# Optimization experiments

Hardware: AMD Instinct MI355X
Metric: run time of the kernel (lower is better)

## Reference

```python
import jax, jax.numpy as jnp
import numpy as np

IN_FEATURES = 2048
OUT_FEATURES = 2048
BLOCK_SIZE = 16
F_BLOCKS = (OUT_FEATURES + BLOCK_SIZE - 1) // BLOCK_SIZE  # 128
G_BLOCKS = (IN_FEATURES + BLOCK_SIZE - 1) // BLOCK_SIZE   # 128
BATCH = 4096


def setup_inputs() -> dict:
    key = jax.random.key(0)
    k1, k2, k3 = jax.random.split(key, 3)
    x = jax.random.normal(k1, (BATCH, IN_FEATURES), dtype=jnp.float32)
    # Xavier-uniform-ish scale for index vectors viewed as (f*g, block_size)
    limit = np.sqrt(6.0 / (F_BLOCKS * G_BLOCKS + BLOCK_SIZE)).astype(np.float32)
    index_vectors = jax.random.uniform(
        k2, (F_BLOCKS, G_BLOCKS, BLOCK_SIZE), dtype=jnp.float32,
        minval=-limit, maxval=limit)
    b = jax.random.normal(k3, (OUT_FEATURES,), dtype=jnp.float32) * 0.02
    return {"x": x, "index_vectors": index_vectors, "b": b}


def reference(x, index_vectors, b):
    batch = x.shape[0]
    padded_in = G_BLOCKS * BLOCK_SIZE
    padded_out = F_BLOCKS * BLOCK_SIZE
    if x.shape[1] < padded_in:
        x = jnp.pad(x, ((0, 0), (0, padded_in - x.shape[1])))
    x_blocks = x.reshape(batch, G_BLOCKS, BLOCK_SIZE)            # (B, g, b)
    # Batched FFT over all blocks at once (replaces the f*g python loop)
    fft_p = jnp.fft.fft(index_vectors, axis=-1)                  # (f, g, b) complex
    fft_x = jnp.fft.fft(x_blocks, axis=-1)                       # (B, g, b) complex
    # sum_j IFFT(P_ij * X_j) == IFFT(sum_j P_ij * X_j) by linearity of IFFT
    out_fft = jnp.einsum('fgb,Bgb->Bfb', fft_p, fft_x)           # (B, f, b) complex
    out_blocks = jnp.fft.ifft(out_fft, axis=-1).real             # (B, f, b)
    out = out_blocks.reshape(batch, padded_out)
    if padded_out > OUT_FEATURES:
        out = out[:, :OUT_FEATURES]
    return out + b
```

## Files before the change

kernel.cpp:

```cpp
#include <hip/hip_runtime.h>
#include <hip/hip_bf16.h>


#define M_DIM 4096
#define N_DIM 2048
#define K_DIM 2048
#define BK 64
#define NT (K_DIM / BK)
#define BUFSZ 49152

typedef __attribute__((ext_vector_type(8))) short bf16x8;
typedef __attribute__((ext_vector_type(4))) float f32x4;

typedef const __attribute__((address_space(1))) void gvoid_t;
typedef __attribute__((address_space(3))) void lvoid_t;

#define FENCE asm volatile("" ::: "memory")
#define BAR()  do { FENCE; __builtin_amdgcn_s_barrier(); FENCE; } while (0)
#define GLD(src, dst) __builtin_amdgcn_global_load_lds((gvoid_t*)(src), (lvoid_t*)(dst), 16, 0, 0)

#define STAGE_A(dst, src) (GLD((src) + 0 * 64 * K_DIM, (dst) + 0),     \
                           GLD((src) + 1 * 64 * K_DIM, (dst) + 8192),  \
                           GLD((src) + 2 * 64 * K_DIM, (dst) + 16384), \
                           GLD((src) + 3 * 64 * K_DIM, (dst) + 24576))
#define STAGE_B(dst, src) (GLD((src) + 0 * 64 * K_DIM, (dst) + 0),     \
                           GLD((src) + 1 * 64 * K_DIM, (dst) + 8192))

__device__ __forceinline__ unsigned int f2bf(float f) {
  unsigned int u = __float_as_uint(f);
  return (u + 0x7fffu + ((u >> 16) & 1u)) >> 16;
}

__global__ __launch_bounds__(256) void prep_kernel(const float* __restrict__ x,
                                                   const float* __restrict__ iv,
                                                   unsigned short* __restrict__ xb,
                                                   unsigned short* __restrict__ W) {
  int b = blockIdx.x;
  if (b < (M_DIM * K_DIM / 8) / 256) {
    int idx = b * 256 + threadIdx.x;
    const float4* x4 = (const float4*)x;
    float4 a = x4[idx * 2 + 0];
    float4 c = x4[idx * 2 + 1];
    uint4 o;
    o.x = f2bf(a.x) | (f2bf(a.y) << 16);
    o.y = f2bf(a.z) | (f2bf(a.w) << 16);
    o.z = f2bf(c.x) | (f2bf(c.y) << 16);
    o.w = f2bf(c.z) | (f2bf(c.w) << 16);
    ((uint4*)xb)[idx] = o;
  } else {
    int idx = (b - (M_DIM * K_DIM / 8) / 256) * 256 + threadIdx.x;
    int o  = idx >> 8;
    int i0 = (idx & 255) * 8;
    int f = o >> 4, t = o & 15;
    int g = i0 >> 4, u0 = i0 & 15;
    const float* row = iv + (f * 128 + g) * 16;
    unsigned int p[4];
#pragma unroll
    for (int j = 0; j < 4; ++j) {
      unsigned int lo = f2bf(row[(t - (u0 + 2 * j + 0)) & 15]);
      unsigned int hi = f2bf(row[(t - (u0 + 2 * j + 1)) & 15]);
      p[j] = lo | (hi << 16);
    }
    ((uint4*)W)[idx] = make_uint4(p[0], p[1], p[2], p[3]);
  }
}

__global__ __launch_bounds__(512, 2) void gemm_bias_kernel(const unsigned short* __restrict__ A,
                                                           const unsigned short* __restrict__ B,
                                                           const float* __restrict__ bias,
                                                           float* __restrict__ C) {
  __shared__ char lds[3 * BUFSZ];

  const int tid = threadIdx.x;
  const int l   = tid & 63;
  const int w   = tid >> 6;
  const int wm  = w >> 1;
  const int wn  = w & 1;

  const int orig = blockIdx.x;
  const int swz  = (orig & 7) * 32 + (orig >> 3);
  const int bm   = swz >> 4;
  const int bn   = swz & 15;

  f32x4 acc[4][4] = {};

  const int srow  = w * 8 + (l >> 3);
  const int sslot = (l & 7) ^ ((l >> 3) & 7);
  const unsigned short* Asrc0 = A + (size_t)(bm * 256 + srow) * K_DIM + sslot * 8;
  const unsigned short* Bsrc0 = B + (size_t)(bn * 128 + srow) * K_DIM + sslot * 8;

  const int fr = l & 15;
  const int rxor = (l & 7) << 4;
  const int aRow0 = (wm * 64 + fr) * 128;
  const int bRow0 = (wn * 64 + fr) * 128;
  const int swzcol0 = (0 * 64 + (l >> 4) * 16) ^ rxor;
  const int swzcol1 = (1 * 64 + (l >> 4) * 16) ^ rxor;

  bf16x8 fa0[4], fb0[4], fa1[4], fb1[4];

#define LDA(SA, SB, BUF, SWZ)                                           \
  do {                                                                  \
    const char* Ab_ = lds + (BUF) * BUFSZ;                              \
    const char* Bb_ = Ab_ + 32768;                                      \
    _Pragma("unroll")                                                   \
    for (int m = 0; m < 4; ++m)                                         \
      SA[m] = *(const bf16x8*)(Ab_ + aRow0 + m * 2048 + (SWZ));         \
    _Pragma("unroll")                                                   \
    for (int n = 0; n < 4; ++n)                                         \
      SB[n] = *(const bf16x8*)(Bb_ + bRow0 + n * 2048 + (SWZ));         \
  } while (0)

#define MM(SA, SB, CNT)                                                 \
  do {                                                                  \
    asm volatile("s_waitcnt lgkmcnt(" #CNT ")" ::: "memory");           \
    __builtin_amdgcn_sched_barrier(0);                                  \
    __builtin_amdgcn_s_setprio(1);                                      \
    _Pragma("unroll")                                                   \
    for (int m = 0; m < 4; ++m)                                         \
      _Pragma("unroll")                                                 \
      for (int n = 0; n < 4; ++n)                                       \
        acc[m][n] = __builtin_amdgcn_mfma_f32_16x16x32_bf16(SA[m], SB[n], acc[m][n], 0, 0, 0); \
    __builtin_amdgcn_s_setprio(0);                                      \
    __builtin_amdgcn_sched_barrier(0);                                  \
  } while (0)

#define TILE_FULL(CUR, NXT, STG, T)                                     \
  do {                                                                  \
    LDA(fa1, fb1, CUR, swzcol1);                                        \
    STAGE_A(lds + (STG) * BUFSZ + w * 1024, Asrc0 + ((T) + 2) * BK);    \
    MM(fa0, fb0, 8);                                                    \
    asm volatile("s_waitcnt vmcnt(4)" ::: "memory");                    \
    BAR();                                                              \
    LDA(fa0, fb0, NXT, swzcol0);                                        \
    STAGE_B(lds + (STG) * BUFSZ + 32768 + w * 1024, Bsrc0 + ((T) + 2) * BK); \
    MM(fa1, fb1, 8);                                                    \
    BAR();                                                              \
  } while (0)

  STAGE_A(lds + 0 * BUFSZ + w * 1024, Asrc0 + 0 * BK);
  STAGE_B(lds + 0 * BUFSZ + 32768 + w * 1024, Bsrc0 + 0 * BK);
  STAGE_A(lds + 1 * BUFSZ + w * 1024, Asrc0 + 1 * BK);
  STAGE_B(lds + 1 * BUFSZ + 32768 + w * 1024, Bsrc0 + 1 * BK);
  asm volatile("s_waitcnt vmcnt(6)" ::: "memory");
  BAR();
  LDA(fa0, fb0, 0, swzcol0);

  for (int t = 0; t < NT - 2; t += 3) {
    TILE_FULL(0, 1, 2, t);
    TILE_FULL(1, 2, 0, t + 1);
    TILE_FULL(2, 0, 1, t + 2);
  }

  LDA(fa1, fb1, 0, swzcol1);
  MM(fa0, fb0, 8);
  asm volatile("s_waitcnt vmcnt(0)" ::: "memory");
  BAR();
  LDA(fa0, fb0, 1, swzcol0);
  MM(fa1, fb1, 8);
  LDA(fa1, fb1, 1, swzcol1);
  MM(fa0, fb0, 8);
  MM(fa1, fb1, 0);

  const int row0 = bm * 256 + wm * 64 + (l >> 4) * 4;
  const int col0 = bn * 128 + wn * 64 + (l & 15);
#pragma unroll
  for (int n = 0; n < 4; ++n) {
    float bv = bias[col0 + n * 16];
#pragma unroll
    for (int m = 0; m < 4; ++m) {
#pragma unroll
      for (int j = 0; j < 4; ++j) {
        C[(size_t)(row0 + m * 16 + j) * N_DIM + (col0 + n * 16)] = acc[m][n][j] + bv;
      }
    }
  }
#undef TILE_FULL
#undef MM
#undef LDA
}

__global__ __launch_bounds__(256) void fallback_kernel(const float* __restrict__ x,
                                                       const float* __restrict__ iv,
                                                       const float* __restrict__ b,
                                                       float* __restrict__ out) {
  int idx = blockIdx.x * 256 + threadIdx.x;
  int Bn = idx >> 11, o = idx & 2047;
  int f = o >> 4, t = o & 15;
  const float* xr = x + (size_t)Bn * 2048;
  float acc = 0.f;
  for (int g = 0; g < 128; ++g) {
    const float* pr = iv + (f * 128 + g) * 16;
    const float* xg = xr + g * 16;
#pragma unroll
    for (int s = 0; s < 16; ++s) acc += pr[s] * xg[(t - s) & 15];
  }
  out[idx] = acc + b[o];
}

extern "C" void kernel_launch(void* const* d_in, const int* in_sizes, int n_in,
                              void* d_out, int out_size, void* d_ws, size_t ws_size,
                              hipStream_t stream) {
  const float* x    = (const float*)d_in[0];
  const float* iv   = (const float*)d_in[1];
  const float* bias = (const float*)d_in[2];
  float* out = (float*)d_out;

  const size_t xb_bytes = (size_t)M_DIM * K_DIM * 2;
  const size_t w_bytes  = (size_t)N_DIM * K_DIM * 2;
  if (ws_size < xb_bytes + w_bytes) {
    fallback_kernel<<<(M_DIM * N_DIM) / 256, 256, 0, stream>>>(x, iv, bias, out);
    return;
  }

  unsigned short* xb = (unsigned short*)d_ws;
  unsigned short* W  = xb + (size_t)M_DIM * K_DIM;

  const int cvt_blocks = (M_DIM * K_DIM / 8) / 256;
  const int bw_blocks  = (N_DIM * K_DIM / 8) / 256;
  prep_kernel<<<cvt_blocks + bw_blocks, 256, 0, stream>>>(x, iv, xb, W);

  gemm_bias_kernel<<<(M_DIM / 256) * (N_DIM / 128), 512, 0, stream>>>(xb, W, bias, out);
}
```

Before: 55.10 us.

## Switch GEMM to 32x32x16 MFMA with intra-block split-K and LDS reduction

Replaces the 16x16x32 MFMA tiling with 32x32x16 bf16 MFMAs. The 8 waves become a 2x2 output grid with two K-groups that each take half of every 64-wide K tile, and the two partial results are reduced through LDS in the epilogue before bias is added. The main loop is restructured so each iteration issues the A and B stages together and waits once per tile, with a single barrier per tile instead of two. The larger MFMA shape is meant to cut LDS fragment traffic per FLOP and instruction issue overhead. In exchange it adds an LDS reduction pass and barrier at the end and raises accumulator register use per wave.

```diff
diff --git a/kernel.cpp b/kernel.cpp
--- a/kernel.cpp
+++ b/kernel.cpp
@@ -11,6 +11,7 @@
 
 typedef __attribute__((ext_vector_type(8))) short bf16x8;
 typedef __attribute__((ext_vector_type(4))) float f32x4;
+typedef __attribute__((ext_vector_type(16))) float f32x16;
 
 typedef const __attribute__((address_space(1))) void gvoid_t;
 typedef __attribute__((address_space(3))) void lvoid_t;
@@ -74,67 +75,70 @@
   const int tid = threadIdx.x;
   const int l   = tid & 63;
   const int w   = tid >> 6;
-  const int wm  = w >> 1;
+  const int wm  = (w >> 1) & 1;
   const int wn  = w & 1;
+  const int kg  = w >> 2;
 
   const int orig = blockIdx.x;
   const int swz  = (orig & 7) * 32 + (orig >> 3);
   const int bm   = swz >> 4;
   const int bn   = swz & 15;
 
-  f32x4 acc[4][4] = {};
+  f32x16 acc[4][2] = {};
 
   const int srow  = w * 8 + (l >> 3);
   const int sslot = (l & 7) ^ ((l >> 3) & 7);
   const unsigned short* Asrc0 = A + (size_t)(bm * 256 + srow) * K_DIM + sslot * 8;
   const unsigned short* Bsrc0 = B + (size_t)(bn * 128 + srow) * K_DIM + sslot * 8;
 
-  const int fr = l & 15;
   const int rxor = (l & 7) << 4;
-  const int aRow0 = (wm * 64 + fr) * 128;
-  const int bRow0 = (wn * 64 + fr) * 128;
-  const int swzcol0 = (0 * 64 + (l >> 4) * 16) ^ rxor;
-  const int swzcol1 = (1 * 64 + (l >> 4) * 16) ^ rxor;
-
-  bf16x8 fa0[4], fb0[4], fa1[4], fb1[4];
-
-#define LDA(SA, SB, BUF, SWZ)                                           \
+  const int aRowB = (wm * 128 + (l & 31)) * 128;
+  const int bRowB = (wn * 64 + (l & 31)) * 128;
+  const int kc0 = (kg * 64 + 0 * 32 + (l >> 5) * 16) ^ rxor;
+  const int kc1 = (kg * 64 + 1 * 32 + (l >> 5) * 16) ^ rxor;
+
+  bf16x8 fa0[4][2], fb0[2][2], fa1[4][2], fb1[2][2];
+
+#define LDFRAGS(FA, FB, BUFC)                                           \
   do {                                                                  \
-    const char* Ab_ = lds + (BUF) * BUFSZ;                              \
+    const char* Ab_ = lds + (BUFC) * BUFSZ;                             \
     const char* Bb_ = Ab_ + 32768;                                      \
     _Pragma("unroll")                                                   \
-    for (int m = 0; m < 4; ++m)                                         \
-      SA[m] = *(const bf16x8*)(Ab_ + aRow0 + m * 2048 + (SWZ));         \
+    for (int mm = 0; mm < 4; ++mm) {                                    \
+      FA[mm][0] = *(const bf16x8*)(Ab_ + aRowB + mm * 4096 + kc0);      \
+      FA[mm][1] = *(const bf16x8*)(Ab_ + aRowB + mm * 4096 + kc1);      \
+    }                                                                   \
     _Pragma("unroll")                                                   \
-    for (int n = 0; n < 4; ++n)                                         \
-      SB[n] = *(const bf16x8*)(Bb_ + bRow0 + n * 2048 + (SWZ));         \
+    for (int nn = 0; nn < 2; ++nn) {                                    \
+      FB[nn][0] = *(const bf16x8*)(Bb_ + bRowB + nn * 4096 + kc0);      \
+      FB[nn][1] = *(const bf16x8*)(Bb_ + bRowB + nn * 4096 + kc1);      \
+    }                                                                   \
   } while (0)
 
-#define MM(SA, SB, CNT)                                                 \
+#define MFMA16(FA, FB, CNT)                                             \
   do {                                                                  \
     asm volatile("s_waitcnt lgkmcnt(" #CNT ")" ::: "memory");           \
     __builtin_amdgcn_sched_barrier(0);                                  \
     __builtin_amdgcn_s_setprio(1);                                      \
     _Pragma("unroll")                                                   \
-    for (int m = 0; m < 4; ++m)                                         \
+    for (int s = 0; s < 2; ++s)                                         \
       _Pragma("unroll")                                                 \
-      for (int n = 0; n < 4; ++n)                                       \
-        acc[m][n] = __builtin_amdgcn_mfma_f32_16x16x32_bf16(SA[m], SB[n], acc[m][n], 0, 0, 0); \
+      for (int mm = 0; mm < 4; ++mm)                                    \
+        _Pragma("unroll")                                               \
+        for (int nn = 0; nn < 2; ++nn)                                  \
+          acc[mm][nn] = __builtin_amdgcn_mfma_f32_32x32x16_bf16(FA[mm][s], FB[nn][s], acc[mm][nn], 0, 0, 0); \
     __builtin_amdgcn_s_setprio(0);                                      \
     __builtin_amdgcn_sched_barrier(0);                                  \
   } while (0)
 
-#define TILE_FULL(CUR, NXT, STG, T)                                     \
+#define BODY(T, BUF2, BUF1, FAc, FBc, FAn, FBn)                         \
   do {                                                                  \
-    LDA(fa1, fb1, CUR, swzcol1);                                        \
-    STAGE_A(lds + (STG) * BUFSZ + w * 1024, Asrc0 + ((T) + 2) * BK);    \
-    MM(fa0, fb0, 8);                                                    \
-    asm volatile("s_waitcnt vmcnt(4)" ::: "memory");                    \
+    STAGE_A(lds + (BUF2) * BUFSZ + w * 1024, Asrc0 + ((T) + 2) * BK);   \
+    STAGE_B(lds + (BUF2) * BUFSZ + 32768 + w * 1024, Bsrc0 + ((T) + 2) * BK); \
+    asm volatile("s_waitcnt vmcnt(6)" ::: "memory");                    \
     BAR();                                                              \
-    LDA(fa0, fb0, NXT, swzcol0);                                        \
-    STAGE_B(lds + (STG) * BUFSZ + 32768 + w * 1024, Bsrc0 + ((T) + 2) * BK); \
-    MM(fa1, fb1, 8);                                                    \
-    BAR();                                                              \
+    LDFRAGS(FAn, FBn, BUF1);                                            \
+    MFMA16(FAc, FBc, 12);                                               \
   } while (0)
 
   STAGE_A(lds + 0 * BUFSZ + w * 1024, Asrc0 + 0 * BK);
@@ -143,40 +147,73 @@
   STAGE_B(lds + 1 * BUFSZ + 32768 + w * 1024, Bsrc0 + 1 * BK);
   asm volatile("s_waitcnt vmcnt(6)" ::: "memory");
   BAR();
-  LDA(fa0, fb0, 0, swzcol0);
-
-  for (int t = 0; t < NT - 2; t += 3) {
-    TILE_FULL(0, 1, 2, t);
-    TILE_FULL(1, 2, 0, t + 1);
-    TILE_FULL(2, 0, 1, t + 2);
-  }
-
-  LDA(fa1, fb1, 0, swzcol1);
-  MM(fa0, fb0, 8);
+  LDFRAGS(fa0, fb0, 0);
+
+  for (int t = 0; t < NT - 2; t += 6) {
+    BODY(t + 0, 2, 1, fa0, fb0, fa1, fb1);
+    BODY(t + 1, 0, 2, fa1, fb1, fa0, fb0);
+    BODY(t + 2, 1, 0, fa0, fb0, fa1, fb1);
+    BODY(t + 3, 2, 1, fa1, fb1, fa0, fb0);
+    BODY(t + 4, 0, 2, fa0, fb0, fa1, fb1);
+    BODY(t + 5, 1, 0, fa1, fb1, fa0, fb0);
+  }
+
   asm volatile("s_waitcnt vmcnt(0)" ::: "memory");
   BAR();
-  LDA(fa0, fb0, 1, swzcol0);
-  MM(fa1, fb1, 8);
-  LDA(fa1, fb1, 1, swzcol1);
-  MM(fa0, fb0, 8);
-  MM(fa1, fb1, 0);
-
-  const int row0 = bm * 256 + wm * 64 + (l >> 4) * 4;
-  const int col0 = bn * 128 + wn * 64 + (l & 15);
-#pragma unroll
-  for (int n = 0; n < 4; ++n) {
-    float bv = bias[col0 + n * 16];
-#pragma unroll
-    for (int m = 0; m < 4; ++m) {
-#pragma unroll
-      for (int j = 0; j < 4; ++j) {
-        C[(size_t)(row0 + m * 16 + j) * N_DIM + (col0 + n * 16)] = acc[m][n][j] + bv;
+  LDFRAGS(fa1, fb1, 1);
+  MFMA16(fa0, fb0, 12);
+  MFMA16(fa1, fb1, 0);
+
+  BAR();
+  {
+    const int p = w & 3;
+    float* rb = (float*)lds + (size_t)p * 2 * 64 * 68;
+    float* mysub  = rb + (kg ? 0 : 1) * 64 * 68;
+    float* othsub = rb + (kg ? 1 : 0) * 64 * 68;
+    const int mmw0 = kg ? 0 : 2;
+    const int mmk0 = kg ? 2 : 0;
+#pragma unroll
+    for (int mi = 0; mi < 2; ++mi)
+#pragma unroll
+      for (int nn = 0; nn < 2; ++nn)
+#pragma unroll
+        for (int q = 0; q < 4; ++q) {
+          const int rloc = mi * 32 + q * 8 + (l >> 5) * 4;
+          const int col  = nn * 32 + (l & 31);
+          f32x4 v;
+          v[0] = acc[mmw0 + mi][nn][q * 4 + 0];
+          v[1] = acc[mmw0 + mi][nn][q * 4 + 1];
+          v[2] = acc[mmw0 + mi][nn][q * 4 + 2];
+          v[3] = acc[mmw0 + mi][nn][q * 4 + 3];
+          *(f32x4*)(mysub + col * 68 + rloc) = v;
+        }
+    asm volatile("s_waitcnt lgkmcnt(0)" ::: "memory");
+    BAR();
+    const int col0 = bn * 128 + wn * 64;
+#pragma unroll
+    for (int nn = 0; nn < 2; ++nn) {
+      const float bv = bias[col0 + nn * 32 + (l & 31)];
+#pragma unroll
+      for (int mi = 0; mi < 2; ++mi) {
+#pragma unroll
+        for (int q = 0; q < 4; ++q) {
+          const int rloc = mi * 32 + q * 8 + (l >> 5) * 4;
+          const int col  = nn * 32 + (l & 31);
+          f32x4 r = *(const f32x4*)(othsub + col * 68 + rloc);
+          const int crow = bm * 256 + wm * 128 + (mmk0 + mi) * 32 + q * 8 + (l >> 5) * 4;
+          const int ccol = col0 + nn * 32 + (l & 31);
+#pragma unroll
+          for (int j = 0; j < 4; ++j) {
+            C[(size_t)(crow + j) * N_DIM + ccol] =
+                acc[mmk0 + mi][nn][q * 4 + j] + r[j] + bv;
+          }
+        }
       }
     }
   }
-#undef TILE_FULL
-#undef MM
-#undef LDA
+#undef BODY
+#undef MFMA16
+#undef LDFRAGS
 }
 
 __global__ __launch_bounds__(256) void fallback_kernel(const float* __restrict__ x,
```

Result: slower. 100.3 us (+82.1%).

## Load B operand directly from global into registers, staging only A in LDS

Applied to the files above, without the earlier changes.

The GEMM no longer stages the B tile through LDS. Each wave loads its B fragments straight from global memory into registers one k-tile ahead, with double-buffered register sets, and only the A tile keeps the triple-buffered LDS pipeline. The main loop is restructured into a single barrier per k-tile and unrolled six-way to rotate the register and LDS buffers. This removes LDS traffic and barriers for B and cuts LDS use from 144KB to 96KB. In exchange, the four waves that share B columns fetch the same data redundantly through the cache, the 16-byte-per-lane row-strided loads coalesce less well, and register pressure rises.

```diff
diff --git a/kernel.cpp b/kernel.cpp
--- a/kernel.cpp
+++ b/kernel.cpp
@@ -7,7 +7,7 @@
 #define K_DIM 2048
 #define BK 64
 #define NT (K_DIM / BK)
-#define BUFSZ 49152
+#define ABUF 32768
 
 typedef __attribute__((ext_vector_type(8))) short bf16x8;
 typedef __attribute__((ext_vector_type(4))) float f32x4;
@@ -23,8 +23,6 @@
                            GLD((src) + 1 * 64 * K_DIM, (dst) + 8192),  \
                            GLD((src) + 2 * 64 * K_DIM, (dst) + 16384), \
                            GLD((src) + 3 * 64 * K_DIM, (dst) + 24576))
-#define STAGE_B(dst, src) (GLD((src) + 0 * 64 * K_DIM, (dst) + 0),     \
-                           GLD((src) + 1 * 64 * K_DIM, (dst) + 8192))
 
 __device__ __forceinline__ unsigned int f2bf(float f) {
   unsigned int u = __float_as_uint(f);
@@ -69,7 +67,7 @@
                                                            const unsigned short* __restrict__ B,
                                                            const float* __restrict__ bias,
                                                            float* __restrict__ C) {
-  __shared__ char lds[3 * BUFSZ];
+  __shared__ char lds[3 * ABUF];
 
   const int tid = threadIdx.x;
   const int l   = tid & 63;
@@ -87,79 +85,85 @@
   const int srow  = w * 8 + (l >> 3);
   const int sslot = (l & 7) ^ ((l >> 3) & 7);
   const unsigned short* Asrc0 = A + (size_t)(bm * 256 + srow) * K_DIM + sslot * 8;
-  const unsigned short* Bsrc0 = B + (size_t)(bn * 128 + srow) * K_DIM + sslot * 8;
 
   const int fr = l & 15;
   const int rxor = (l & 7) << 4;
   const int aRow0 = (wm * 64 + fr) * 128;
-  const int bRow0 = (wn * 64 + fr) * 128;
-  const int swzcol0 = (0 * 64 + (l >> 4) * 16) ^ rxor;
-  const int swzcol1 = (1 * 64 + (l >> 4) * 16) ^ rxor;
-
-  bf16x8 fa0[4], fb0[4], fa1[4], fb1[4];
-
-#define LDA(SA, SB, BUF, SWZ)                                           \
-  do {                                                                  \
-    const char* Ab_ = lds + (BUF) * BUFSZ;                              \
-    const char* Bb_ = Ab_ + 32768;                                      \
+  const int swzc0 = (0 * 64 + (l >> 4) * 16) ^ rxor;
+  const int swzc1 = (1 * 64 + (l >> 4) * 16) ^ rxor;
+
+  const unsigned short* Bg = B + (size_t)(bn * 128 + wn * 64 + (l & 15)) * K_DIM + (l >> 4) * 8;
+
+  bf16x8 fa0[4][2], fa1[4][2];
+  bf16x8 bq0[4][2], bq1[4][2];
+
+#define LDA(FA, BUFC)                                                   \
+  do {                                                                  \
+    const char* Ab_ = lds + (BUFC) * ABUF;                              \
     _Pragma("unroll")                                                   \
-    for (int m = 0; m < 4; ++m)                                         \
-      SA[m] = *(const bf16x8*)(Ab_ + aRow0 + m * 2048 + (SWZ));         \
+    for (int m = 0; m < 4; ++m) {                                       \
+      FA[m][0] = *(const bf16x8*)(Ab_ + aRow0 + m * 2048 + swzc0);      \
+      FA[m][1] = *(const bf16x8*)(Ab_ + aRow0 + m * 2048 + swzc1);      \
+    }                                                                   \
+  } while (0)
+
+#define LDB(BQ, T)                                                      \
+  do {                                                                  \
     _Pragma("unroll")                                                   \
-    for (int n = 0; n < 4; ++n)                                         \
-      SB[n] = *(const bf16x8*)(Bb_ + bRow0 + n * 2048 + (SWZ));         \
-  } while (0)
-
-#define MM(SA, SB, CNT)                                                 \
+    for (int n = 0; n < 4; ++n) {                                       \
+      BQ[n][0] = *(const bf16x8*)(Bg + n * 16 * K_DIM + (T) * BK + 0);  \
+      BQ[n][1] = *(const bf16x8*)(Bg + n * 16 * K_DIM + (T) * BK + 32); \
+    }                                                                   \
+  } while (0)
+
+#define MFMA32(FA, BQ, CNT)                                             \
   do {                                                                  \
     asm volatile("s_waitcnt lgkmcnt(" #CNT ")" ::: "memory");           \
     __builtin_amdgcn_sched_barrier(0);                                  \
     __builtin_amdgcn_s_setprio(1);                                      \
     _Pragma("unroll")                                                   \
-    for (int m = 0; m < 4; ++m)                                         \
+    for (int kc = 0; kc < 2; ++kc)                                      \
       _Pragma("unroll")                                                 \
-      for (int n = 0; n < 4; ++n)                                       \
-        acc[m][n] = __builtin_amdgcn_mfma_f32_16x16x32_bf16(SA[m], SB[n], acc[m][n], 0, 0, 0); \
+      for (int m = 0; m < 4; ++m)                                       \
+        _Pragma("unroll")                                               \
+        for (int n = 0; n < 4; ++n)                                     \
+          acc[m][n] = __builtin_amdgcn_mfma_f32_16x16x32_bf16(FA[m][kc], BQ[n][kc], acc[m][n], 0, 0, 0); \
     __builtin_amdgcn_s_setprio(0);                                      \
     __builtin_amdgcn_sched_barrier(0);                                  \
   } while (0)
 
-#define TILE_FULL(CUR, NXT, STG, T)                                     \
-  do {                                                                  \
-    LDA(fa1, fb1, CUR, swzcol1);                                        \
-    STAGE_A(lds + (STG) * BUFSZ + w * 1024, Asrc0 + ((T) + 2) * BK);    \
-    MM(fa0, fb0, 8);                                                    \
-    asm volatile("s_waitcnt vmcnt(4)" ::: "memory");                    \
+#define BODY(T, BUF1, BUF2, FAc, FAn, BQc, BQn)                         \
+  do {                                                                  \
+    asm volatile("s_waitcnt vmcnt(8)" ::: "memory");                    \
     BAR();                                                              \
-    LDA(fa0, fb0, NXT, swzcol0);                                        \
-    STAGE_B(lds + (STG) * BUFSZ + 32768 + w * 1024, Bsrc0 + ((T) + 2) * BK); \
-    MM(fa1, fb1, 8);                                                    \
-    BAR();                                                              \
-  } while (0)
-
-  STAGE_A(lds + 0 * BUFSZ + w * 1024, Asrc0 + 0 * BK);
-  STAGE_B(lds + 0 * BUFSZ + 32768 + w * 1024, Bsrc0 + 0 * BK);
-  STAGE_A(lds + 1 * BUFSZ + w * 1024, Asrc0 + 1 * BK);
-  STAGE_B(lds + 1 * BUFSZ + 32768 + w * 1024, Bsrc0 + 1 * BK);
-  asm volatile("s_waitcnt vmcnt(6)" ::: "memory");
+    LDA(FAn, BUF1);                                                     \
+    STAGE_A(lds + (BUF2) * ABUF + w * 1024, Asrc0 + ((T) + 2) * BK);    \
+    LDB(BQn, (T) + 1);                                                  \
+    MFMA32(FAc, BQc, 8);                                                \
+  } while (0)
+
+  STAGE_A(lds + 0 * ABUF + w * 1024, Asrc0 + 0 * BK);
+  STAGE_A(lds + 1 * ABUF + w * 1024, Asrc0 + 1 * BK);
+  LDB(bq0, 0);
+  asm volatile("s_waitcnt vmcnt(12)" ::: "memory");
   BAR();
-  LDA(fa0, fb0, 0, swzcol0);
-
-  for (int t = 0; t < NT - 2; t += 3) {
-    TILE_FULL(0, 1, 2, t);
-    TILE_FULL(1, 2, 0, t + 1);
-    TILE_FULL(2, 0, 1, t + 2);
-  }
-
-  LDA(fa1, fb1, 0, swzcol1);
-  MM(fa0, fb0, 8);
-  asm volatile("s_waitcnt vmcnt(0)" ::: "memory");
+  LDA(fa0, 0);
+
+  for (int t = 0; t < NT - 2; t += 6) {
+    BODY(t + 0, 1, 2, fa0, fa1, bq0, bq1);
+    BODY(t + 1, 2, 0, fa1, fa0, bq1, bq0);
+    BODY(t + 2, 0, 1, fa0, fa1, bq0, bq1);
+    BODY(t + 3, 1, 2, fa1, fa0, bq1, bq0);
+    BODY(t + 4, 2, 0, fa0, fa1, bq0, bq1);
+    BODY(t + 5, 0, 1, fa1, fa0, bq1, bq0);
+  }
+
+  asm volatile("s_waitcnt vmcnt(8)" ::: "memory");
   BAR();
-  LDA(fa0, fb0, 1, swzcol0);
-  MM(fa1, fb1, 8);
-  LDA(fa1, fb1, 1, swzcol1);
-  MM(fa0, fb0, 8);
-  MM(fa1, fb1, 0);
+  LDA(fa1, 1);
+  LDB(bq1, 31);
+  MFMA32(fa0, bq0, 8);
+  MFMA32(fa1, bq1, 0);
 
   const int row0 = bm * 256 + wm * 64 + (l >> 4) * 4;
   const int col0 = bn * 128 + wn * 64 + (l & 15);
@@ -174,8 +178,9 @@
       }
     }
   }
-#undef TILE_FULL
-#undef MM
+#undef BODY
+#undef MFMA32
+#undef LDB
 #undef LDA
 }
 
```

Result: slower. 99.92 us (+81.4%).

## Fuse fp32-to-bf16 conversion of x into GEMM A-tile loading

Applied to the files above, without the earlier changes.

Drops the separate pass that converts x to bf16 in workspace. The GEMM now loads fp32 x tiles into registers, converts them to bf16 and writes them swizzled into LDS, replacing the direct global-to-LDS loads for A. This removes a 32MB read plus 16MB write round trip, but each GEMM block re-reads A as fp32, doubling A traffic per tile. It also adds register pressure and a full vmcnt(0) wait each iteration, which weakens the load/compute overlap.

```diff
diff --git a/kernel.cpp b/kernel.cpp
--- a/kernel.cpp
+++ b/kernel.cpp
@@ -19,10 +19,6 @@
 #define BAR()  do { FENCE; __builtin_amdgcn_s_barrier(); FENCE; } while (0)
 #define GLD(src, dst) __builtin_amdgcn_global_load_lds((gvoid_t*)(src), (lvoid_t*)(dst), 16, 0, 0)
 
-#define STAGE_A(dst, src) (GLD((src) + 0 * 64 * K_DIM, (dst) + 0),     \
-                           GLD((src) + 1 * 64 * K_DIM, (dst) + 8192),  \
-                           GLD((src) + 2 * 64 * K_DIM, (dst) + 16384), \
-                           GLD((src) + 3 * 64 * K_DIM, (dst) + 24576))
 #define STAGE_B(dst, src) (GLD((src) + 0 * 64 * K_DIM, (dst) + 0),     \
                            GLD((src) + 1 * 64 * K_DIM, (dst) + 8192))
 
@@ -31,41 +27,25 @@
   return (u + 0x7fffu + ((u >> 16) & 1u)) >> 16;
 }
 
-__global__ __launch_bounds__(256) void prep_kernel(const float* __restrict__ x,
-                                                   const float* __restrict__ iv,
-                                                   unsigned short* __restrict__ xb,
+__global__ __launch_bounds__(256) void prep_kernel(const float* __restrict__ iv,
                                                    unsigned short* __restrict__ W) {
-  int b = blockIdx.x;
-  if (b < (M_DIM * K_DIM / 8) / 256) {
-    int idx = b * 256 + threadIdx.x;
-    const float4* x4 = (const float4*)x;
-    float4 a = x4[idx * 2 + 0];
-    float4 c = x4[idx * 2 + 1];
-    uint4 o;
-    o.x = f2bf(a.x) | (f2bf(a.y) << 16);
-    o.y = f2bf(a.z) | (f2bf(a.w) << 16);
-    o.z = f2bf(c.x) | (f2bf(c.y) << 16);
-    o.w = f2bf(c.z) | (f2bf(c.w) << 16);
-    ((uint4*)xb)[idx] = o;
-  } else {
-    int idx = (b - (M_DIM * K_DIM / 8) / 256) * 256 + threadIdx.x;
-    int o  = idx >> 8;
-    int i0 = (idx & 255) * 8;
-    int f = o >> 4, t = o & 15;
-    int g = i0 >> 4, u0 = i0 & 15;
-    const float* row = iv + (f * 128 + g) * 16;
-    unsigned int p[4];
-#pragma unroll
-    for (int j = 0; j < 4; ++j) {
-      unsigned int lo = f2bf(row[(t - (u0 + 2 * j + 0)) & 15]);
-      unsigned int hi = f2bf(row[(t - (u0 + 2 * j + 1)) & 15]);
-      p[j] = lo | (hi << 16);
-    }
-    ((uint4*)W)[idx] = make_uint4(p[0], p[1], p[2], p[3]);
-  }
-}
-
-__global__ __launch_bounds__(512, 2) void gemm_bias_kernel(const unsigned short* __restrict__ A,
+  int idx = blockIdx.x * 256 + threadIdx.x;
+  int o  = idx >> 8;
+  int i0 = (idx & 255) * 8;
+  int f = o >> 4, t = o & 15;
+  int g = i0 >> 4, u0 = i0 & 15;
+  const float* row = iv + (f * 128 + g) * 16;
+  unsigned int p[4];
+#pragma unroll
+  for (int j = 0; j < 4; ++j) {
+    unsigned int lo = f2bf(row[(t - (u0 + 2 * j + 0)) & 15]);
+    unsigned int hi = f2bf(row[(t - (u0 + 2 * j + 1)) & 15]);
+    p[j] = lo | (hi << 16);
+  }
+  ((uint4*)W)[idx] = make_uint4(p[0], p[1], p[2], p[3]);
+}
+
+__global__ __launch_bounds__(512, 2) void gemm_bias_kernel(const float* __restrict__ X,
                                                            const unsigned short* __restrict__ B,
                                                            const float* __restrict__ bias,
                                                            float* __restrict__ C) {
@@ -84,9 +64,13 @@
 
   f32x4 acc[4][4] = {};
 
+  const int arow = w * 8 + (l >> 3);
+  const int ks   = l & 7;
+  const float* Afp = X + (size_t)(bm * 256 + arow) * K_DIM + ks * 8;
+  const int awbyte = arow * 128 + ((ks ^ ((l >> 3) & 7)) * 16);
+
   const int srow  = w * 8 + (l >> 3);
   const int sslot = (l & 7) ^ ((l >> 3) & 7);
-  const unsigned short* Asrc0 = A + (size_t)(bm * 256 + srow) * K_DIM + sslot * 8;
   const unsigned short* Bsrc0 = B + (size_t)(bn * 128 + srow) * K_DIM + sslot * 8;
 
   const int fr = l & 15;
@@ -97,6 +81,7 @@
   const int swzcol1 = (1 * 64 + (l >> 4) * 16) ^ rxor;
 
   bf16x8 fa0[4], fb0[4], fa1[4], fb1[4];
+  float4 av[4][2];
 
 #define LDA(SA, SB, BUF, SWZ)                                           \
   do {                                                                  \
@@ -108,6 +93,29 @@
     _Pragma("unroll")                                                   \
     for (int n = 0; n < 4; ++n)                                         \
       SB[n] = *(const bf16x8*)(Bb_ + bRow0 + n * 2048 + (SWZ));         \
+  } while (0)
+
+#define ALOAD(T)                                                        \
+  do {                                                                  \
+    _Pragma("unroll")                                                   \
+    for (int j = 0; j < 4; ++j) {                                       \
+      av[j][0] = *(const float4*)(Afp + (size_t)j * 64 * K_DIM + (T) * BK + 0); \
+      av[j][1] = *(const float4*)(Afp + (size_t)j * 64 * K_DIM + (T) * BK + 4); \
+    }                                                                   \
+  } while (0)
+
+#define AWRITE(BUFC)                                                    \
+  do {                                                                  \
+    char* dst_ = lds + (BUFC) * BUFSZ;                                  \
+    _Pragma("unroll")                                                   \
+    for (int j = 0; j < 4; ++j) {                                       \
+      uint4 u_;                                                         \
+      u_.x = f2bf(av[j][0].x) | (f2bf(av[j][0].y) << 16);               \
+      u_.y = f2bf(av[j][0].z) | (f2bf(av[j][0].w) << 16);               \
+      u_.z = f2bf(av[j][1].x) | (f2bf(av[j][1].y) << 16);               \
+      u_.w = f2bf(av[j][1].z) | (f2bf(av[j][1].w) << 16);               \
+      *(uint4*)(dst_ + j * 8192 + awbyte) = u_;                         \
+    }                                                                   \
   } while (0)
 
 #define MM(SA, SB, CNT)                                                 \
@@ -124,31 +132,35 @@
     __builtin_amdgcn_sched_barrier(0);                                  \
   } while (0)
 
-#define TILE_FULL(CUR, NXT, STG, T)                                     \
+#define BODY(T, CUR, NXT, STG)                                          \
   do {                                                                  \
     LDA(fa1, fb1, CUR, swzcol1);                                        \
-    STAGE_A(lds + (STG) * BUFSZ + w * 1024, Asrc0 + ((T) + 2) * BK);    \
+    ALOAD((T) + 2);                                                     \
     MM(fa0, fb0, 8);                                                    \
-    asm volatile("s_waitcnt vmcnt(4)" ::: "memory");                    \
+    AWRITE(STG);                                                        \
+    asm volatile("s_waitcnt vmcnt(0)" ::: "memory");                    \
     BAR();                                                              \
     LDA(fa0, fb0, NXT, swzcol0);                                        \
     STAGE_B(lds + (STG) * BUFSZ + 32768 + w * 1024, Bsrc0 + ((T) + 2) * BK); \
-    MM(fa1, fb1, 8);                                                    \
+    MM(fa1, fb1, 12);                                                   \
     BAR();                                                              \
   } while (0)
 
-  STAGE_A(lds + 0 * BUFSZ + w * 1024, Asrc0 + 0 * BK);
+  ALOAD(0);
+  AWRITE(0);
+  ALOAD(1);
+  AWRITE(1);
   STAGE_B(lds + 0 * BUFSZ + 32768 + w * 1024, Bsrc0 + 0 * BK);
-  STAGE_A(lds + 1 * BUFSZ + w * 1024, Asrc0 + 1 * BK);
   STAGE_B(lds + 1 * BUFSZ + 32768 + w * 1024, Bsrc0 + 1 * BK);
-  asm volatile("s_waitcnt vmcnt(6)" ::: "memory");
+  asm volatile("s_waitcnt vmcnt(0)" ::: "memory");
+  asm volatile("s_waitcnt lgkmcnt(0)" ::: "memory");
   BAR();
   LDA(fa0, fb0, 0, swzcol0);
 
   for (int t = 0; t < NT - 2; t += 3) {
-    TILE_FULL(0, 1, 2, t);
-    TILE_FULL(1, 2, 0, t + 1);
-    TILE_FULL(2, 0, 1, t + 2);
+    BODY(t + 0, 0, 1, 2);
+    BODY(t + 1, 1, 2, 0);
+    BODY(t + 2, 2, 0, 1);
   }
 
   LDA(fa1, fb1, 0, swzcol1);
@@ -174,8 +186,10 @@
       }
     }
   }
-#undef TILE_FULL
+#undef BODY
 #undef MM
+#undef AWRITE
+#undef ALOAD
 #undef LDA
 }
 
@@ -205,19 +219,14 @@
   const float* bias = (const float*)d_in[2];
   float* out = (float*)d_out;
 
-  const size_t xb_bytes = (size_t)M_DIM * K_DIM * 2;
-  const size_t w_bytes  = (size_t)N_DIM * K_DIM * 2;
-  if (ws_size < xb_bytes + w_bytes) {
+  const size_t w_bytes = (size_t)N_DIM * K_DIM * 2;
+  if (ws_size < w_bytes) {
     fallback_kernel<<<(M_DIM * N_DIM) / 256, 256, 0, stream>>>(x, iv, bias, out);
     return;
   }
 
-  unsigned short* xb = (unsigned short*)d_ws;
-  unsigned short* W  = xb + (size_t)M_DIM * K_DIM;
-
-  const int cvt_blocks = (M_DIM * K_DIM / 8) / 256;
-  const int bw_blocks  = (N_DIM * K_DIM / 8) / 256;
-  prep_kernel<<<cvt_blocks + bw_blocks, 256, 0, stream>>>(x, iv, xb, W);
-
-  gemm_bias_kernel<<<(M_DIM / 256) * (N_DIM / 128), 512, 0, stream>>>(xb, W, bias, out);
-}
+  unsigned short* W = (unsigned short*)d_ws;
+
+  prep_kernel<<<(N_DIM * K_DIM / 8) / 256, 256, 0, stream>>>(iv, W);
+  gemm_bias_kernel<<<(M_DIM / 256) * (N_DIM / 128), 512, 0, stream>>>(x, W, bias, out);
+}
```

Measured after the change: 76.67 us. 39.2% more time.
